# Kernel tuning notes

Hardware: AMD Instinct MI355X
Metric: run time of the kernel (lower is better)

## Reference

```python
import jax, jax.numpy as jnp
import numpy as np

B, N, DIM, H, DH = 4, 2048, 512, 8, 64  # patches_num == N (required by the math)
INNER = H * DH
SCALE = DH ** -0.5


def setup_inputs() -> dict:
    key = jax.random.key(0)
    ks = jax.random.split(key, 6)
    s = lambda fan_in: 1.0 / np.sqrt(fan_in)
    return {
        "x": jax.random.normal(ks[0], (B, N, DIM), dtype=jnp.float32),
        "w_qkfv": jax.random.normal(ks[1], (DIM, 4 * INNER), dtype=jnp.float32) * s(DIM),
        "w_scales": jax.random.normal(ks[2], (DH, N), dtype=jnp.float32) * s(DH),
        "b_scales": jax.random.normal(ks[3], (N,), dtype=jnp.float32) * s(DH),
        "w_out": jax.random.normal(ks[4], (INNER, DIM), dtype=jnp.float32) * s(INNER),
        "b_out": jax.random.normal(ks[5], (DIM,), dtype=jnp.float32) * s(INNER),
    }


def reference(x, w_qkfv, w_scales, b_scales, w_out, b_out):
    # Fused qkfv projection: [B,N,4*INNER]
    qkfv = x @ w_qkfv
    q, k, f, v = jnp.split(qkfv, 4, axis=-1)
    split_heads = lambda t: t.reshape(B, N, H, DH).transpose(0, 2, 1, 3)  # b h n d
    q, k, f, v = map(split_heads, (q, k, f, v))

    # q @ k^T * scale -> [b,h,n,n]
    scores = jnp.einsum("bhid,bhjd->bhij", q, k) * SCALE
    attn = jax.nn.softmax(scores, axis=-1)

    # f^T @ v -> [b,h,d,d], then Linear(dim_head -> patches_num) -> [b,h,d,n]
    poss_value = jnp.einsum("bhnd,bhne->bhde", f, v)
    poss_value = poss_value @ w_scales + b_scales  # [b,h,d,n]

    # attn @ poss_value^T -> [b,h,n,d]
    out = jnp.einsum("bhij,bhdj->bhid", attn, poss_value)
    out = out.transpose(0, 2, 1, 3).reshape(B, N, INNER)  # b n (h d)

    # to_out (dropout=0 / eval mode -> identity)
    return out @ w_out + b_out
```

## Files before the change

kernel.cpp:

```cpp
#include <hip/hip_runtime.h>
#include <stdint.h>

#define N_SEQ 2048
#define QKFV_COLS 2048

typedef __attribute__((ext_vector_type(8))) __bf16 bf16x8;
typedef __attribute__((ext_vector_type(4))) __bf16 bf16x4;
typedef __attribute__((ext_vector_type(4))) float f32x4;
typedef __attribute__((ext_vector_type(16))) float f32x16;

#if __has_builtin(__builtin_amdgcn_exp2f)
#define EXP2(x) __builtin_amdgcn_exp2f(x)
#else
#define EXP2(x) exp2f(x)
#endif

__device__ __forceinline__ f32x4 mfma16(bf16x8 a, bf16x8 b, f32x4 c) {
  return __builtin_amdgcn_mfma_f32_16x16x32_bf16(a, b, c, 0, 0, 0);
}
__device__ __forceinline__ f32x16 mfma32(bf16x8 a, bf16x8 b, f32x16 c) {
  return __builtin_amdgcn_mfma_f32_32x32x16_bf16(a, b, c, 0, 0, 0);
}

__device__ __forceinline__ void glds16(const void* g, void* l) {
  __builtin_amdgcn_global_load_lds(
      (__attribute__((address_space(1))) uint32_t*)(uintptr_t)g,
      (__attribute__((address_space(3))) uint32_t*)l, 16, 0, 0);
}

__global__ __launch_bounds__(256) void cast_bf16_kernel(const float* __restrict__ in,
                                                        __bf16* __restrict__ out, int n8) {
  int i = blockIdx.x * 256 + threadIdx.x;
  if (i >= n8) return;
  const float* p = in + (size_t)i * 8;
  bf16x8 o;
#pragma unroll
  for (int j = 0; j < 8; ++j) o[j] = (__bf16)p[j];
  *(bf16x8*)(out + (size_t)i * 8) = o;
}

__global__ __launch_bounds__(256) void transpose_cast_kernel(const float* __restrict__ in,
                                                             __bf16* __restrict__ out,
                                                             int R, int C) {
  int i = blockIdx.x * 256 + threadIdx.x;
  int nchunks = C * (R / 8);
  if (i >= nchunks) return;
  int c = i / (R / 8);
  int r0 = (i % (R / 8)) * 8;
  bf16x8 o;
#pragma unroll
  for (int j = 0; j < 8; ++j) o[j] = (__bf16)in[(size_t)(r0 + j) * C + c];
  *(bf16x8*)(out + (size_t)c * R + r0) = o;
}

template<typename OUT_T, bool BIAS>
__global__ __launch_bounds__(256) void gemm_bt_kernel(const __bf16* __restrict__ A,
                                                      const __bf16* __restrict__ Bt,
                                                      OUT_T* __restrict__ C,
                                                      const float* __restrict__ bias,
                                                      int M, int N, int K) {
  __shared__ alignas(16) __bf16 As[128 * 32];
  __shared__ alignas(16) __bf16 Bs[128 * 32];
  const int t = threadIdx.x;
  const int w = t >> 6;
  const int lane = t & 63;
  const int ln = lane & 15;
  const int hi8 = (lane >> 4) * 8;
  const int g4 = (lane >> 4) * 4;
  const int wr = w >> 1, wc = w & 1;
  const int m0 = blockIdx.x * 128, n0 = blockIdx.y * 128;

  f32x4 acc[4][4];
#pragma unroll
  for (int m = 0; m < 4; ++m)
#pragma unroll
    for (int n = 0; n < 4; ++n) acc[m][n] = (f32x4){0.f, 0.f, 0.f, 0.f};

  const int nk = K >> 5;
  for (int kt = 0; kt < nk; ++kt) {
    const int k0 = kt << 5;
#pragma unroll
    for (int i = 0; i < 2; ++i) {
      int c = i * 256 + t;
      int r = c >> 2, cc = c & 3;
      glds16(A + (size_t)(m0 + r) * K + k0 + cc * 8, &As[(i * 256 + w * 64) * 8]);
      glds16(Bt + (size_t)(n0 + r) * K + k0 + cc * 8, &Bs[(i * 256 + w * 64) * 8]);
    }
    __syncthreads();
    bf16x8 af[4], bfr[4];
#pragma unroll
    for (int m = 0; m < 4; ++m) af[m] = *(const bf16x8*)&As[(wr * 64 + m * 16 + ln) * 32 + hi8];
#pragma unroll
    for (int n = 0; n < 4; ++n) bfr[n] = *(const bf16x8*)&Bs[(wc * 64 + n * 16 + ln) * 32 + hi8];
#pragma unroll
    for (int m = 0; m < 4; ++m)
#pragma unroll
      for (int n = 0; n < 4; ++n) acc[m][n] = mfma16(af[m], bfr[n], acc[m][n]);
    __syncthreads();
  }

#pragma unroll
  for (int m = 0; m < 4; ++m)
#pragma unroll
    for (int n = 0; n < 4; ++n) {
      int col = n0 + wc * 64 + n * 16 + ln;
      float bv = BIAS ? bias[col] : 0.f;
#pragma unroll
      for (int r = 0; r < 4; ++r) {
        int row = m0 + wr * 64 + m * 16 + g4 + r;
        C[(size_t)row * N + col] = (OUT_T)(acc[m][n][r] + bv);
      }
    }
}

__global__ __launch_bounds__(512, 2) void gemm256_kernel(const __bf16* __restrict__ A,
                                                         const __bf16* __restrict__ Bt,
                                                         __bf16* __restrict__ C,
                                                         int M, int N, int K) {
  __shared__ alignas(16) __bf16 Ab[2][256 * 64];
  __shared__ alignas(16) __bf16 Bb[2][256 * 64];
  const int t = threadIdx.x;
  const int w = t >> 6;
  const int lane = t & 63;
  const int l15 = lane & 15;
  const int q4 = lane >> 4;
  const int g4 = q4 * 4;
  const int wr = w >> 2, wc = w & 3;
  const int bid = blockIdx.x;
  const int wg = (bid & 7) * 32 + (bid >> 3);
  const int m0 = (wg & 31) * 256;
  const int n0 = (wg >> 5) * 256;

  const __bf16* srcA[4];
  const __bf16* srcB[4];
#pragma unroll
  for (int c = 0; c < 4; ++c) {
    int s = c * 512 + t;
    int r = s >> 3, u = (s & 7) ^ (r & 7);
    srcA[c] = A + (size_t)(m0 + r) * K + u * 8;
    srcB[c] = Bt + (size_t)(n0 + r) * K + u * 8;
  }

  f32x4 acc[8][4];
#pragma unroll
  for (int m = 0; m < 8; ++m)
#pragma unroll
    for (int n = 0; n < 4; ++n) acc[m][n] = (f32x4){0.f, 0.f, 0.f, 0.f};

  const int sA = l15 & 7;

#pragma unroll
  for (int c = 0; c < 4; ++c) {
    glds16(srcA[c], &Ab[0][(c * 512 + w * 64) * 8]);
    glds16(srcB[c], &Bb[0][(c * 512 + w * 64) * 8]);
  }

  const int nkt = K >> 6;
  for (int kt = 0; kt < nkt; ++kt) {
    const int cur = kt & 1;
    asm volatile("s_waitcnt vmcnt(0)" ::: "memory");
    __builtin_amdgcn_s_barrier();
    const int knext = (kt + 1) << 6;
    const bool pf = (kt + 1) < nkt;
#pragma unroll
    for (int mh = 0; mh < 2; ++mh) {
      bf16x8 a[4][2];
#pragma unroll
      for (int nh = 0; nh < 2; ++nh) {
        if (nh == 0) {
#pragma unroll
          for (int mm = 0; mm < 4; ++mm) {
            const int R = wr * 128 + (mh * 4 + mm) * 16 + l15;
#pragma unroll
            for (int ks = 0; ks < 2; ++ks)
              a[mm][ks] = *(const bf16x8*)&Ab[cur][R * 64 + (((ks * 4 + q4) ^ sA) * 8)];
          }
        }
        bf16x8 bfrag[2][2];
#pragma unroll
        for (int nn = 0; nn < 2; ++nn) {
          const int R = wc * 64 + (nh * 2 + nn) * 16 + l15;
#pragma unroll
          for (int ks = 0; ks < 2; ++ks)
            bfrag[nn][ks] = *(const bf16x8*)&Bb[cur][R * 64 + (((ks * 4 + q4) ^ sA) * 8)];
        }
        if (pf) {
          const int c = mh * 2 + nh;
          glds16(srcA[c] + knext, &Ab[cur ^ 1][(c * 512 + w * 64) * 8]);
          glds16(srcB[c] + knext, &Bb[cur ^ 1][(c * 512 + w * 64) * 8]);
        }
        __builtin_amdgcn_s_barrier();
        asm volatile("s_waitcnt lgkmcnt(0)" ::: "memory");
        __builtin_amdgcn_sched_barrier(0);
        __builtin_amdgcn_s_setprio(1);
#pragma unroll
        for (int mm = 0; mm < 4; ++mm)
#pragma unroll
          for (int nn = 0; nn < 2; ++nn)
#pragma unroll
            for (int ks = 0; ks < 2; ++ks)
              acc[mh * 4 + mm][nh * 2 + nn] =
                  mfma16(a[mm][ks], bfrag[nn][ks], acc[mh * 4 + mm][nh * 2 + nn]);
        __builtin_amdgcn_s_setprio(0);
        __builtin_amdgcn_s_barrier();
      }
    }
  }

#pragma unroll
  for (int m = 0; m < 8; ++m)
#pragma unroll
    for (int n = 0; n < 4; ++n) {
      const int col = n0 + wc * 64 + n * 16 + l15;
      const int row = m0 + wr * 128 + m * 16 + g4;
#pragma unroll
      for (int r = 0; r < 4; ++r)
        C[(size_t)(row + r) * N + col] = (__bf16)acc[m][n][r];
    }
}

__global__ __launch_bounds__(256) void fv_kernel(const __bf16* __restrict__ qkfv,
                                                 float* __restrict__ fvp) {
  __shared__ alignas(16) float Ft[64 * 64];
  __shared__ alignas(16) float Vt[64 * 64];
  const int t = threadIdx.x;
  const int bh = blockIdx.y;
  const int b = bh >> 3, h = bh & 7;
  const int n0 = blockIdx.x * 128;
  const int d = t >> 2;
  const int e0 = (t & 3) * 16;
  f32x4 acc[4];
#pragma unroll
  for (int k = 0; k < 4; ++k) acc[k] = (f32x4){0.f, 0.f, 0.f, 0.f};

  for (int tile = 0; tile < 2; ++tile) {
    const int nb = n0 + tile * 64;
    __syncthreads();
#pragma unroll
    for (int i = 0; i < 2; ++i) {
      int c = i * 256 + t;
      int r = c >> 3, cc = c & 7;
      const size_t rowbase = (size_t)(b * N_SEQ + nb + r) * QKFV_COLS + h * 64 + cc * 8;
      bf16x8 f8 = *(const bf16x8*)(qkfv + rowbase + 1024);
      bf16x8 v8 = *(const bf16x8*)(qkfv + rowbase + 1536);
#pragma unroll
      for (int j = 0; j < 8; ++j) {
        Ft[r * 64 + cc * 8 + j] = (float)f8[j];
        Vt[r * 64 + cc * 8 + j] = (float)v8[j];
      }
    }
    __syncthreads();
    for (int nn = 0; nn < 64; ++nn) {
      float fd = Ft[nn * 64 + d];
#pragma unroll
      for (int k = 0; k < 4; ++k)
        acc[k] += fd * *(const f32x4*)&Vt[nn * 64 + e0 + k * 4];
    }
  }
  float* dst = fvp + (size_t)blockIdx.x * 131072 + (size_t)bh * 4096 + d * 64 + e0;
#pragma unroll
  for (int k = 0; k < 4; ++k)
    *(f32x4*)(dst + k * 4) = acc[k];
}

__global__ __launch_bounds__(256) void fvreduce_kernel(const float* __restrict__ fvp,
                                                       float* __restrict__ fvb) {
  int i = blockIdx.x * 256 + threadIdx.x;
  float s = 0.f;
#pragma unroll
  for (int p = 0; p < 16; ++p) s += fvp[(size_t)p * 131072 + i];
  fvb[i] = s;
}

__global__ __launch_bounds__(256) void pvmat_kernel(const float* __restrict__ fvb,
                                                    const float* __restrict__ wsc,
                                                    const float* __restrict__ bsc,
                                                    __bf16* __restrict__ pvm) {
  __shared__ alignas(16) float fvs[64 * 65];
  __shared__ alignas(16) float wst[64 * 128];
  const int t = threadIdx.x;
  const int bh = blockIdx.y;
  const int j0 = blockIdx.x * 128;
#pragma unroll
  for (int i = 0; i < 16; ++i) {
    int idx = i * 256 + t;
    fvs[(idx >> 6) * 65 + (idx & 63)] = fvb[(size_t)bh * 4096 + idx];
  }
#pragma unroll
  for (int i = 0; i < 8; ++i) {
    int c = i * 256 + t;
    int e = c >> 5, cc = c & 31;
    *(f32x4*)&wst[e * 128 + cc * 4] = *(const f32x4*)&wsc[(size_t)e * 2048 + j0 + cc * 4];
  }
  __syncthreads();
  const int d0 = (t >> 3) * 2;
  const int jb = (t & 7) * 4;
  f32x4 acc[2][4];
#pragma unroll
  for (int dd = 0; dd < 2; ++dd)
#pragma unroll
    for (int k4 = 0; k4 < 4; ++k4)
#pragma unroll
      for (int x = 0; x < 4; ++x)
        acc[dd][k4][x] = bsc[j0 + jb + k4 * 32 + x];
  for (int e = 0; e < 64; ++e) {
    float f0 = fvs[d0 * 65 + e];
    float f1 = fvs[(d0 + 1) * 65 + e];
#pragma unroll
    for (int k4 = 0; k4 < 4; ++k4) {
      f32x4 wv = *(const f32x4*)&wst[e * 128 + jb + k4 * 32];
      acc[0][k4] += f0 * wv;
      acc[1][k4] += f1 * wv;
    }
  }
#pragma unroll
  for (int dd = 0; dd < 2; ++dd) {
    __bf16* dst = pvm + (size_t)bh * 64 * 2048 + (size_t)(d0 + dd) * 2048 + j0;
#pragma unroll
    for (int k4 = 0; k4 < 4; ++k4)
#pragma unroll
      for (int x = 0; x < 4; ++x)
        dst[jb + k4 * 32 + x] = (__bf16)acc[dd][k4][x];
  }
}

__global__ __launch_bounds__(512, 4) void attn_kernel(const __bf16* __restrict__ qkfv,
                                                      const __bf16* __restrict__ pvm,
                                                      __bf16* __restrict__ obuf) {
  __shared__ alignas(16) char smem[65536];
  __bf16* Kb = (__bf16*)smem;
  __bf16* Vb = (__bf16*)(smem + 32768);
  const int t = threadIdx.x;
  const int w = t >> 6;
  const int g = w >> 2;
  const int wq = w & 3;
  const int lane = t & 63;
  const int ln = lane & 31;
  const int hi = lane >> 5;
  const int p = blockIdx.x;
  const int bh = (p & 7) * 4 + ((p >> 3) & 3);
  const int iblk = p >> 5;
  const int b = bh >> 3, h = bh & 7;
  const int irow = iblk * 128 + wq * 32 + ln;
  const float K1 = 0.18033688f;
  const int swz = ln & 7;

  bf16x8 q[4];
  const __bf16* qrow = qkfv + (size_t)(b * N_SEQ + irow) * QKFV_COLS + h * 64 + hi * 8;
#pragma unroll
  for (int kf = 0; kf < 4; ++kf) {
    bf16x8 raw = *(const bf16x8*)(qrow + kf * 16);
#pragma unroll
    for (int e = 0; e < 8; ++e) q[kf][e] = (__bf16)((float)raw[e] * K1);
  }

  const int tg = t & 255;
  const __bf16* ksrc[2];
  const __bf16* vsrc[2];
#pragma unroll
  for (int it = 0; it < 2; ++it) {
    int s = it * 256 + tg;
    int r = s >> 3;
    int u = (s & 7) ^ (r & 7);
    ksrc[it] = qkfv + (size_t)(b * N_SEQ + g * 1024 + r) * QKFV_COLS + 512 + h * 64 + u * 8;
    vsrc[it] = pvm + ((size_t)bh * 64 + r) * 2048 + g * 1024 + u * 8;
  }

  auto stage = [&](int buf, int jt) {
#pragma unroll
    for (int it = 0; it < 2; ++it) {
      glds16(ksrc[it] + ((size_t)jt << 17), &Kb[(g * 2 + buf) * 4096 + (it * 256 + wq * 64) * 8]);
      glds16(vsrc[it] + jt * 64, &Vb[(g * 2 + buf) * 4096 + (it * 256 + wq * 64) * 8]);
    }
  };

  f32x16 o0, o1;
#pragma unroll
  for (int e = 0; e < 16; ++e) { o0[e] = 0.f; o1[e] = 0.f; }
  float lrl = 0.f;

  stage(0, 0);

  for (int jt = 0; jt < 16; ++jt) {
    asm volatile("s_waitcnt vmcnt(0)" ::: "memory");
    __builtin_amdgcn_s_barrier();
    if (jt < 15) stage((jt & 1) ^ 1, jt + 1);
    const int kc = (g * 2 + (jt & 1)) * 4096;

    f32x16 s0, s1;
#pragma unroll
    for (int e = 0; e < 16; ++e) { s0[e] = 0.f; s1[e] = 0.f; }
    __builtin_amdgcn_s_setprio(1);
#pragma unroll
    for (int kf = 0; kf < 4; ++kf) {
      bf16x8 k0 = *(const bf16x8*)&Kb[kc + (ln) * 64 + (((2 * kf + hi) ^ swz) * 8)];
      bf16x8 k1 = *(const bf16x8*)&Kb[kc + (32 + ln) * 64 + (((2 * kf + hi) ^ swz) * 8)];
      s0 = mfma32(k0, q[kf], s0);
      s1 = mfma32(k1, q[kf], s1);
    }
    __builtin_amdgcn_s_setprio(0);

#pragma unroll
    for (int e = 0; e < 16; ++e) s0[e] = EXP2(s0[e]);
#pragma unroll
    for (int e = 0; e < 16; ++e) s1[e] = EXP2(s1[e]);
    float a8[8];
#pragma unroll
    for (int e = 0; e < 8; ++e)
      a8[e] = (s0[e] + s0[e + 8]) + (s1[e] + s1[e + 8]);
    lrl += ((a8[0] + a8[4]) + (a8[1] + a8[5])) + ((a8[2] + a8[6]) + (a8[3] + a8[7]));

    bf16x8 pa[4];
#pragma unroll
    for (int kk = 0; kk < 4; ++kk) {
      const f32x16& sf = (kk < 2) ? s0 : s1;
      const int rb = (kk & 1) * 8;
      uint32_t a0, a1, b0, b1;
      asm("v_cvt_pk_bf16_f32 %0, %1, %2" : "=v"(a0) : "v"(sf[rb + 0]), "v"(sf[rb + 1]));
      asm("v_cvt_pk_bf16_f32 %0, %1, %2" : "=v"(a1) : "v"(sf[rb + 2]), "v"(sf[rb + 3]));
      asm("v_cvt_pk_bf16_f32 %0, %1, %2" : "=v"(b0) : "v"(sf[rb + 4]), "v"(sf[rb + 5]));
      asm("v_cvt_pk_bf16_f32 %0, %1, %2" : "=v"(b1) : "v"(sf[rb + 6]), "v"(sf[rb + 7]));
      asm("v_permlane32_swap_b32 %0, %1" : "+v"(a0), "+v"(b0));
      asm("v_permlane32_swap_b32 %0, %1" : "+v"(a1), "+v"(b1));
      union { uint32_t u[4]; bf16x8 v; } cv;
      cv.u[0] = a0; cv.u[1] = a1; cv.u[2] = b0; cv.u[3] = b1;
      pa[kk] = cv.v;
    }

    __builtin_amdgcn_s_setprio(1);
#pragma unroll
    for (int kk = 0; kk < 4; ++kk) {
      bf16x8 v0 = *(const bf16x8*)&Vb[kc + (ln) * 64 + (((2 * kk + hi) ^ swz) * 8)];
      bf16x8 v1 = *(const bf16x8*)&Vb[kc + (32 + ln) * 64 + (((2 * kk + hi) ^ swz) * 8)];
      o0 = mfma32(v0, pa[kk], o0);
      o1 = mfma32(v1, pa[kk], o1);
    }
    __builtin_amdgcn_s_setprio(0);
  }

  lrl += __shfl_xor(lrl, 32);

  __syncthreads();
  float* Om = (float*)smem;
  if (w >= 4) {
    const int base = ((w - 4) * 64 + lane) * 33;
#pragma unroll
    for (int e = 0; e < 16; ++e) { Om[base + e] = o0[e]; Om[base + 16 + e] = o1[e]; }
    Om[base + 32] = lrl;
  }
  __syncthreads();
  if (w < 4) {
    const int base = (w * 64 + lane) * 33;
#pragma unroll
    for (int e = 0; e < 16; ++e) { o0[e] += Om[base + e]; o1[e] += Om[base + 16 + e]; }
    lrl += Om[base + 32];

    const float inv = 1.0f / lrl;
    const size_t orow = (size_t)(b * N_SEQ + irow) * 512 + h * 64;
#pragma unroll
    for (int df = 0; df < 2; ++df) {
      const f32x16& oo = df ? o1 : o0;
#pragma unroll
      for (int gg = 0; gg < 4; ++gg) {
        bf16x4 pk;
#pragma unroll
        for (int e = 0; e < 4; ++e) pk[e] = (__bf16)(oo[gg * 4 + e] * inv);
        *(bf16x4*)(obuf + orow + df * 32 + gg * 8 + hi * 4) = pk;
      }
    }
  }
}

extern "C" void kernel_launch(void* const* d_in, const int* in_sizes, int n_in,
                              void* d_out, int out_size, void* d_ws, size_t ws_size,
                              hipStream_t stream) {
  (void)in_sizes; (void)n_in; (void)out_size; (void)ws_size;
  const float* x   = (const float*)d_in[0];
  const float* wqk = (const float*)d_in[1];
  const float* wsc = (const float*)d_in[2];
  const float* bsc = (const float*)d_in[3];
  const float* wo  = (const float*)d_in[4];
  const float* bo  = (const float*)d_in[5];
  float* out = (float*)d_out;

  char* p = (char*)d_ws;
  __bf16* xbf  = (__bf16*)p;  p += (size_t)8192 * 512 * 2;
  __bf16* wqT  = (__bf16*)p;  p += (size_t)2048 * 512 * 2;
  __bf16* woT  = (__bf16*)p;  p += (size_t)512 * 512 * 2;
  __bf16* qkfv = (__bf16*)p;  p += (size_t)8192 * 2048 * 2;
  float*  fvb  = (float*)p;   p += (size_t)32 * 4096 * 4;
  __bf16* pvm  = (__bf16*)p;  p += (size_t)32 * 64 * 2048 * 2;
  __bf16* obuf = (__bf16*)p;  p += (size_t)8192 * 512 * 2;
  float* fvp = (float*)xbf;

  cast_bf16_kernel<<<dim3(2048), dim3(256), 0, stream>>>(x, xbf, 8192 * 512 / 8);
  transpose_cast_kernel<<<dim3(512), dim3(256), 0, stream>>>(wqk, wqT, 512, 2048);
  transpose_cast_kernel<<<dim3(128), dim3(256), 0, stream>>>(wo, woT, 512, 512);
  gemm256_kernel<<<dim3(256), dim3(512), 0, stream>>>(xbf, wqT, qkfv, 8192, 2048, 512);
  fv_kernel<<<dim3(16, 32), dim3(256), 0, stream>>>(qkfv, fvp);
  fvreduce_kernel<<<dim3(512), dim3(256), 0, stream>>>(fvp, fvb);
  pvmat_kernel<<<dim3(16, 32), dim3(256), 0, stream>>>(fvb, wsc, bsc, pvm);
  attn_kernel<<<dim3(512), dim3(512), 0, stream>>>(qkfv, pvm, obuf);
  gemm_bt_kernel<float, true><<<dim3(64, 4), dim3(256), 0, stream>>>(obuf, woT, out, bo, 8192, 512, 512);
}
```

Baseline: 133.9 us.

## Write f/v transposed from QKFV GEMM and compute fv and pvmat with MFMA

The QKFV GEMM epilogue now writes the f and v columns directly into per-head transposed buffers, laid out so the f^T·v reduction can run as an MFMA GEMM with swizzled LDS tiles instead of a scalar FP32 loop. The separate reduce kernel is folded into the pvmat stage, which now also uses bf16 MFMA against a pre-transposed w_scales. This cuts one launch and the scalar FP32 compute, but adds a transpose launch and extra bf16 rounding of the f·v product. Workspace buffers (obuf, pvm) are reused as scratch for the transposed f and v.

```diff
diff --git a/kernel.cpp b/kernel.cpp
--- a/kernel.cpp
+++ b/kernel.cpp
@@ -116,9 +116,11 @@
 __global__ __launch_bounds__(512, 2) void gemm256_kernel(const __bf16* __restrict__ A,
                                                          const __bf16* __restrict__ Bt,
                                                          __bf16* __restrict__ C,
-                                                         int M, int N, int K) {
+                                                         __bf16* __restrict__ fT,
+                                                         __bf16* __restrict__ vT) {
   __shared__ alignas(16) __bf16 Ab[2][256 * 64];
   __shared__ alignas(16) __bf16 Bb[2][256 * 64];
+  const int K = 512, N = 2048;
   const int t = threadIdx.x;
   const int w = t >> 6;
   const int lane = t & 63;
@@ -207,121 +209,148 @@
     }
   }
 
-#pragma unroll
-  for (int m = 0; m < 8; ++m)
-#pragma unroll
-    for (int n = 0; n < 4; ++n) {
-      const int col = n0 + wc * 64 + n * 16 + l15;
-      const int row = m0 + wr * 128 + m * 16 + g4;
-#pragma unroll
-      for (int r = 0; r < 4; ++r)
-        C[(size_t)(row + r) * N + col] = (__bf16)acc[m][n][r];
-    }
-}
-
-__global__ __launch_bounds__(256) void fv_kernel(const __bf16* __restrict__ qkfv,
-                                                 float* __restrict__ fvp) {
-  __shared__ alignas(16) float Ft[64 * 64];
-  __shared__ alignas(16) float Vt[64 * 64];
+  if (n0 < 1024) {
+#pragma unroll
+    for (int m = 0; m < 8; ++m)
+#pragma unroll
+      for (int n = 0; n < 4; ++n) {
+        const int col = n0 + wc * 64 + n * 16 + l15;
+        const int row = m0 + wr * 128 + m * 16 + g4;
+#pragma unroll
+        for (int r = 0; r < 4; ++r)
+          C[(size_t)(row + r) * N + col] = (__bf16)acc[m][n][r];
+      }
+  } else {
+    __bf16* T = (n0 < 1536) ? fT : vT;
+    const int cbase = (n0 < 1536) ? 1024 : 1536;
+#pragma unroll
+    for (int m = 0; m < 8; ++m)
+#pragma unroll
+      for (int n = 0; n < 4; ++n) {
+        const int hc = n0 + wc * 64 + n * 16 + l15 - cbase;
+        const int h = hc >> 6, d = hc & 63;
+        const int row = m0 + wr * 128 + m * 16 + g4;
+        const int b = row >> 11, nl = row & 2047;
+        bf16x4 pk;
+#pragma unroll
+        for (int r = 0; r < 4; ++r) pk[r] = (__bf16)acc[m][n][r];
+        *(bf16x4*)&T[(size_t)((b * 8 + h) * 64 + d) * 2048 + nl] = pk;
+      }
+  }
+}
+
+__global__ __launch_bounds__(256) void fvmm_kernel(const __bf16* __restrict__ fT,
+                                                   const __bf16* __restrict__ vT,
+                                                   float* __restrict__ fvp) {
+  __shared__ alignas(16) __bf16 As[2 * 8192];
+  __shared__ alignas(16) __bf16 Bs[2 * 8192];
   const int t = threadIdx.x;
+  const int w = t >> 6;
+  const int lane = t & 63;
+  const int l15 = lane & 15;
+  const int q4 = lane >> 4;
+  const int g4 = q4 * 4;
+  const int sl = blockIdx.x;
   const int bh = blockIdx.y;
-  const int b = bh >> 3, h = bh & 7;
-  const int n0 = blockIdx.x * 128;
-  const int d = t >> 2;
-  const int e0 = (t & 3) * 16;
+  const int k0 = sl * 256;
+  const __bf16* A = fT + (size_t)bh * 131072 + k0;
+  const __bf16* B = vT + (size_t)bh * 131072 + k0;
+
+#pragma unroll
+  for (int kt = 0; kt < 2; ++kt)
+#pragma unroll
+    for (int c = 0; c < 4; ++c) {
+      int slot = c * 256 + t;
+      int r = slot >> 4, u = (slot & 15) ^ (r & 7);
+      glds16(A + (size_t)r * 2048 + kt * 128 + u * 8, &As[kt * 8192 + (c * 256 + w * 64) * 8]);
+      glds16(B + (size_t)r * 2048 + kt * 128 + u * 8, &Bs[kt * 8192 + (c * 256 + w * 64) * 8]);
+    }
+  asm volatile("s_waitcnt vmcnt(0)" ::: "memory");
+  __syncthreads();
+
   f32x4 acc[4];
 #pragma unroll
-  for (int k = 0; k < 4; ++k) acc[k] = (f32x4){0.f, 0.f, 0.f, 0.f};
-
-  for (int tile = 0; tile < 2; ++tile) {
-    const int nb = n0 + tile * 64;
-    __syncthreads();
-#pragma unroll
-    for (int i = 0; i < 2; ++i) {
-      int c = i * 256 + t;
-      int r = c >> 3, cc = c & 7;
-      const size_t rowbase = (size_t)(b * N_SEQ + nb + r) * QKFV_COLS + h * 64 + cc * 8;
-      bf16x8 f8 = *(const bf16x8*)(qkfv + rowbase + 1024);
-      bf16x8 v8 = *(const bf16x8*)(qkfv + rowbase + 1536);
-#pragma unroll
-      for (int j = 0; j < 8; ++j) {
-        Ft[r * 64 + cc * 8 + j] = (float)f8[j];
-        Vt[r * 64 + cc * 8 + j] = (float)v8[j];
-      }
-    }
-    __syncthreads();
-    for (int nn = 0; nn < 64; ++nn) {
-      float fd = Ft[nn * 64 + d];
-#pragma unroll
-      for (int k = 0; k < 4; ++k)
-        acc[k] += fd * *(const f32x4*)&Vt[nn * 64 + e0 + k * 4];
-    }
-  }
-  float* dst = fvp + (size_t)blockIdx.x * 131072 + (size_t)bh * 4096 + d * 64 + e0;
-#pragma unroll
-  for (int k = 0; k < 4; ++k)
-    *(f32x4*)(dst + k * 4) = acc[k];
-}
-
-__global__ __launch_bounds__(256) void fvreduce_kernel(const float* __restrict__ fvp,
-                                                       float* __restrict__ fvb) {
-  int i = blockIdx.x * 256 + threadIdx.x;
-  float s = 0.f;
-#pragma unroll
-  for (int p = 0; p < 16; ++p) s += fvp[(size_t)p * 131072 + i];
-  fvb[i] = s;
-}
-
-__global__ __launch_bounds__(256) void pvmat_kernel(const float* __restrict__ fvb,
-                                                    const float* __restrict__ wsc,
-                                                    const float* __restrict__ bsc,
-                                                    __bf16* __restrict__ pvm) {
-  __shared__ alignas(16) float fvs[64 * 65];
-  __shared__ alignas(16) float wst[64 * 128];
+  for (int nb = 0; nb < 4; ++nb) acc[nb] = (f32x4){0.f, 0.f, 0.f, 0.f};
+  const int arow = w * 16 + l15;
+#pragma unroll
+  for (int ks = 0; ks < 8; ++ks) {
+    const int kt = ks >> 2;
+    const int ku = (ks & 3) * 4 + q4;
+    bf16x8 a = *(const bf16x8*)&As[kt * 8192 + arow * 128 + ((ku ^ (arow & 7)) * 8)];
+#pragma unroll
+    for (int nb = 0; nb < 4; ++nb) {
+      const int br = nb * 16 + l15;
+      bf16x8 bb = *(const bf16x8*)&Bs[kt * 8192 + br * 128 + ((ku ^ (br & 7)) * 8)];
+      acc[nb] = mfma16(a, bb, acc[nb]);
+    }
+  }
+  float* dst = fvp + (size_t)(sl * 32 + bh) * 4096;
+#pragma unroll
+  for (int nb = 0; nb < 4; ++nb)
+#pragma unroll
+    for (int r = 0; r < 4; ++r)
+      dst[(w * 16 + g4 + r) * 64 + nb * 16 + l15] = acc[nb][r];
+}
+
+__global__ __launch_bounds__(256) void pvmat2_kernel(const float* __restrict__ fvp,
+                                                     const __bf16* __restrict__ wscT,
+                                                     const float* __restrict__ bsc,
+                                                     __bf16* __restrict__ pvm) {
+  __shared__ alignas(16) __bf16 fs[64 * 72];
+  __shared__ alignas(16) __bf16 Ws[128 * 64];
   const int t = threadIdx.x;
+  const int w = t >> 6;
+  const int lane = t & 63;
+  const int l15 = lane & 15;
+  const int q4 = lane >> 4;
+  const int g4 = q4 * 4;
   const int bh = blockIdx.y;
   const int j0 = blockIdx.x * 128;
-#pragma unroll
-  for (int i = 0; i < 16; ++i) {
-    int idx = i * 256 + t;
-    fvs[(idx >> 6) * 65 + (idx & 63)] = fvb[(size_t)bh * 4096 + idx];
-  }
-#pragma unroll
-  for (int i = 0; i < 8; ++i) {
-    int c = i * 256 + t;
-    int e = c >> 5, cc = c & 31;
-    *(f32x4*)&wst[e * 128 + cc * 4] = *(const f32x4*)&wsc[(size_t)e * 2048 + j0 + cc * 4];
-  }
+
+#pragma unroll
+  for (int c = 0; c < 4; ++c) {
+    int slot = c * 256 + t;
+    int r = slot >> 3, u = (slot & 7) ^ (r & 7);
+    glds16(wscT + (size_t)(j0 + r) * 64 + u * 8, &Ws[(c * 256 + w * 64) * 8]);
+  }
+#pragma unroll
+  for (int qq = 0; qq < 4; ++qq) {
+    int idx = t * 16 + qq * 4;
+    f32x4 s = (f32x4){0.f, 0.f, 0.f, 0.f};
+#pragma unroll
+    for (int sl = 0; sl < 8; ++sl)
+      s += *(const f32x4*)&fvp[(size_t)(sl * 32 + bh) * 4096 + idx];
+    bf16x4 pk;
+#pragma unroll
+    for (int e = 0; e < 4; ++e) pk[e] = (__bf16)s[e];
+    *(bf16x4*)&fs[(idx >> 6) * 72 + (idx & 63)] = pk;
+  }
+  asm volatile("s_waitcnt vmcnt(0)" ::: "memory");
   __syncthreads();
-  const int d0 = (t >> 3) * 2;
-  const int jb = (t & 7) * 4;
-  f32x4 acc[2][4];
-#pragma unroll
-  for (int dd = 0; dd < 2; ++dd)
-#pragma unroll
-    for (int k4 = 0; k4 < 4; ++k4)
-#pragma unroll
-      for (int x = 0; x < 4; ++x)
-        acc[dd][k4][x] = bsc[j0 + jb + k4 * 32 + x];
-  for (int e = 0; e < 64; ++e) {
-    float f0 = fvs[d0 * 65 + e];
-    float f1 = fvs[(d0 + 1) * 65 + e];
-#pragma unroll
-    for (int k4 = 0; k4 < 4; ++k4) {
-      f32x4 wv = *(const f32x4*)&wst[e * 128 + jb + k4 * 32];
-      acc[0][k4] += f0 * wv;
-      acc[1][k4] += f1 * wv;
-    }
-  }
-#pragma unroll
-  for (int dd = 0; dd < 2; ++dd) {
-    __bf16* dst = pvm + (size_t)bh * 64 * 2048 + (size_t)(d0 + dd) * 2048 + j0;
-#pragma unroll
-    for (int k4 = 0; k4 < 4; ++k4)
-#pragma unroll
-      for (int x = 0; x < 4; ++x)
-        dst[jb + k4 * 32 + x] = (__bf16)acc[dd][k4][x];
-  }
+
+  f32x4 acc[8];
+#pragma unroll
+  for (int nb = 0; nb < 8; ++nb) {
+    float bv = bsc[j0 + nb * 16 + l15];
+    acc[nb] = (f32x4){bv, bv, bv, bv};
+  }
+  const int arow = w * 16 + l15;
+#pragma unroll
+  for (int ks = 0; ks < 2; ++ks) {
+    bf16x8 a = *(const bf16x8*)&fs[arow * 72 + ks * 32 + q4 * 8];
+#pragma unroll
+    for (int nb = 0; nb < 8; ++nb) {
+      const int jr = nb * 16 + l15;
+      bf16x8 bb = *(const bf16x8*)&Ws[jr * 64 + (((ks * 4 + q4) ^ (jr & 7)) * 8)];
+      acc[nb] = mfma16(a, bb, acc[nb]);
+    }
+  }
+  __bf16* dst = pvm + (size_t)bh * 131072 + (size_t)j0;
+#pragma unroll
+  for (int nb = 0; nb < 8; ++nb)
+#pragma unroll
+    for (int r = 0; r < 4; ++r)
+      dst[(size_t)(w * 16 + g4 + r) * 2048 + nb * 16 + l15] = (__bf16)acc[nb][r];
 }
 
 __global__ __launch_bounds__(512, 4) void attn_kernel(const __bf16* __restrict__ qkfv,
@@ -487,19 +516,21 @@
   __bf16* xbf  = (__bf16*)p;  p += (size_t)8192 * 512 * 2;
   __bf16* wqT  = (__bf16*)p;  p += (size_t)2048 * 512 * 2;
   __bf16* woT  = (__bf16*)p;  p += (size_t)512 * 512 * 2;
+  __bf16* wscT = (__bf16*)p;  p += (size_t)2048 * 64 * 2;
   __bf16* qkfv = (__bf16*)p;  p += (size_t)8192 * 2048 * 2;
-  float*  fvb  = (float*)p;   p += (size_t)32 * 4096 * 4;
   __bf16* pvm  = (__bf16*)p;  p += (size_t)32 * 64 * 2048 * 2;
   __bf16* obuf = (__bf16*)p;  p += (size_t)8192 * 512 * 2;
   float* fvp = (float*)xbf;
+  __bf16* fT = obuf;
+  __bf16* vT = pvm;
 
   cast_bf16_kernel<<<dim3(2048), dim3(256), 0, stream>>>(x, xbf, 8192 * 512 / 8);
   transpose_cast_kernel<<<dim3(512), dim3(256), 0, stream>>>(wqk, wqT, 512, 2048);
   transpose_cast_kernel<<<dim3(128), dim3(256), 0, stream>>>(wo, woT, 512, 512);
-  gemm256_kernel<<<dim3(256), dim3(512), 0, stream>>>(xbf, wqT, qkfv, 8192, 2048, 512);
-  fv_kernel<<<dim3(16, 32), dim3(256), 0, stream>>>(qkfv, fvp);
-  fvreduce_kernel<<<dim3(512), dim3(256), 0, stream>>>(fvp, fvb);
-  pvmat_kernel<<<dim3(16, 32), dim3(256), 0, stream>>>(fvb, wsc, bsc, pvm);
+  transpose_cast_kernel<<<dim3(64), dim3(256), 0, stream>>>(wsc, wscT, 64, 2048);
+  gemm256_kernel<<<dim3(256), dim3(512), 0, stream>>>(xbf, wqT, qkfv, fT, vT);
+  fvmm_kernel<<<dim3(8, 32), dim3(256), 0, stream>>>(fT, vT, fvp);
+  pvmat2_kernel<<<dim3(16, 32), dim3(256), 0, stream>>>(fvp, wscT, bsc, pvm);
   attn_kernel<<<dim3(512), dim3(512), 0, stream>>>(qkfv, pvm, obuf);
   gemm_bt_kernel<float, true><<<dim3(64, 4), dim3(256), 0, stream>>>(obuf, woT, out, bo, 8192, 512, 512);
 }
```

Measured after the change: 126.8 us. 1.06x faster.
